# Optimization experiments

Measured on AMD Instinct MI355X. Metric: run time of the kernel, lower is better.

## Reference

```python
import jax, jax.numpy as jnp
import numpy as np

TOPK = 6
E = 512
IN = 384
M = 8192
LN_EPS = 1e-5


def _lin(x, w, b):
    # torch nn.Linear: y = x @ W^T + b, W is [out, in]
    return x @ w.T + b


def setup_inputs() -> dict:
    key = jax.random.key(0)
    ks = jax.random.split(key, 16)
    s = lambda k, sh: (jax.random.normal(k, sh, dtype=jnp.float32) * 0.02)
    return {
        "x": jax.random.normal(ks[0], (1, M, IN), dtype=jnp.float32),
        "fc1_w": s(ks[1], (E, IN)), "fc1_b": jnp.zeros((E,), jnp.float32),
        "wh_w": s(ks[2], (E, E)),   "wh_b": jnp.zeros((E,), jnp.float32),
        "wt_w": s(ks[3], (E, E)),   "wt_b": jnp.zeros((E,), jnp.float32),
        "l1_w": s(ks[4], (E, E)),   "l1_b": jnp.zeros((E,), jnp.float32),
        "l2_w": s(ks[5], (E, E)),   "l2_b": jnp.zeros((E,), jnp.float32),
        "a1_w": s(ks[6], (E // 2, E)), "a1_b": jnp.zeros((E // 2,), jnp.float32),
        "a2_w": s(ks[7], (1, E // 2)), "a2_b": jnp.zeros((1,), jnp.float32),
        "ln_g": jnp.ones((E,), jnp.float32), "ln_b": jnp.zeros((E,), jnp.float32),
    }


def reference(x, fc1_w, fc1_b, wh_w, wh_b, wt_w, wt_b,
              l1_w, l1_b, l2_w, l2_b, a1_w, a1_b, a2_w, a2_b, ln_g, ln_b):
    lrelu = jax.nn.leaky_relu  # slope 0.01 == torch default
    h = lrelu(_lin(x, fc1_w, fc1_b))                      # [B,M,E]
    h = (h + h.mean(axis=1, keepdims=True)) * 0.5
    e_h = _lin(h, wh_w, wh_b)                             # [B,M,E]
    e_t = _lin(h, wt_w, wt_b)                             # [B,M,E]
    scale = E ** (-0.5)
    attn_logit = (e_h * scale) @ jnp.swapaxes(e_t, -2, -1)  # [B,M,M]
    topk_weight, topk_index = jax.lax.top_k(attn_logit, TOPK)  # [B,M,K]
    # gather top-k neighbor tail embeddings: [B,M,K,E]
    Nb_h = jax.vmap(lambda et, idx: et[idx])(e_t, topk_index)
    topk_prob = jax.nn.softmax(topk_weight, axis=2)       # [B,M,K]
    eh_r = topk_prob[..., None] * Nb_h + (1.0 - topk_prob)[..., None] * e_h[:, :, None, :]
    gate = jnp.tanh(e_h[:, :, None, :] + eh_r)            # [B,M,K,E]
    # faithful to torch einsum('ijkl,ijkm->ijk'): sums l and m independently
    ka_weight = Nb_h.sum(axis=-1) * gate.sum(axis=-1)     # [B,M,K]
    ka_prob = jax.nn.softmax(ka_weight, axis=2)           # [B,M,K]
    e_Nh = jnp.einsum('bmk,bmke->bme', ka_prob, Nb_h)     # [B,M,E]
    sum_emb = lrelu(_lin(e_h + e_Nh, l1_w, l1_b))
    bi_emb = lrelu(_lin(e_h * e_Nh, l2_w, l2_b))
    emb = sum_emb + bi_emb                                # [B,M,E] (dropout = eval identity)
    hn = emb[0]                                           # squeeze(0) -> [M,E]
    # GeoGlobalAttention readout: gate_nn = Linear->LeakyReLU->Linear, softmax over nodes
    g = _lin(lrelu(_lin(hn, a1_w, a1_b)), a2_w, a2_b)     # [M,1]
    att = jax.nn.softmax(g, axis=0)
    pooled = (att * hn).sum(axis=0, keepdims=True)        # [1,E]
    mu = pooled.mean(axis=-1, keepdims=True)
    var = jnp.mean((pooled - mu) ** 2, axis=-1, keepdims=True)
    out = (pooled - mu) / jnp.sqrt(var + LN_EPS) * ln_g + ln_b
    return out
```

## Files before the change

kernel.cpp:

```cpp
#include <hip/hip_runtime.h>
#include <math.h>
#include <stdint.h>

#define M_NODES 8192
#define E_DIM   512
#define NTOPK   6
#define ATTN_SCALE 0.04419417382415922f
#define NEG_BIG (-1e38f)
#define CAND_CAP 192

typedef __attribute__((ext_vector_type(8))) short short8;
typedef __attribute__((ext_vector_type(4))) float f32x4;

__device__ __forceinline__ float lrelu(float v) { return v > 0.f ? v : 0.01f * v; }

__device__ __forceinline__ unsigned short f2bf(float f) {
  uint32_t u = __float_as_uint(f);
  uint32_t r = (u + 0x7FFFu + ((u >> 16) & 1u)) >> 16;
  return (unsigned short)r;
}
__device__ __forceinline__ float bf2f(unsigned short s) {
  return __uint_as_float(((uint32_t)s) << 16);
}

__device__ __forceinline__ void async_cp16(const void* gptr, void* lds) {
  auto g1 = reinterpret_cast<const __attribute__((address_space(1))) unsigned int*>(
      reinterpret_cast<uintptr_t>(gptr));
  auto l3 = reinterpret_cast<__attribute__((address_space(3))) unsigned int*>(
      reinterpret_cast<uintptr_t>(lds));
  __builtin_amdgcn_global_load_lds(g1, l3, 16, 0, 0);
}


__global__ __launch_bounds__(256) void wcast_kernel(
    const float* __restrict__ x, const float* __restrict__ fc1w,
    const float* __restrict__ whw, const float* __restrict__ wtw,
    const float* __restrict__ l1w, const float* __restrict__ l2w,
    const float* __restrict__ a1w,
    unsigned short* __restrict__ xT, unsigned short* __restrict__ fc1T,
    unsigned short* __restrict__ whT, unsigned short* __restrict__ wtT,
    unsigned short* __restrict__ l1T, unsigned short* __restrict__ l2T,
    unsigned short* __restrict__ a1T)
{
  const int gid = blockIdx.x * 256 + threadIdx.x;
  const float* src; unsigned short* dst; int K8, local;
  if (gid < 417792) {
    K8 = 48;
    if (gid < 393216) { src = x; dst = xT; local = gid; }
    else { src = fc1w; dst = fc1T; local = gid - 393216; }
  } else {
    K8 = 64;
    if (gid < 450560)      { src = whw; dst = whT; local = gid - 417792; }
    else if (gid < 483328) { src = wtw; dst = wtT; local = gid - 450560; }
    else if (gid < 516096) { src = l1w; dst = l1T; local = gid - 483328; }
    else if (gid < 548864) { src = l2w; dst = l2T; local = gid - 516096; }
    else                   { src = a1w; dst = a1T; local = gid - 548864; }
  }
  const int m = local / K8;
  const int k8 = local - m * K8;
  const float* p = src + (size_t)m * (K8 * 8) + k8 * 8;
  float4 v0 = ((const float4*)p)[0];
  float4 v1 = ((const float4*)p)[1];
  const int Kt = K8 >> 2;
  const size_t ti = ((size_t)(m >> 4) * Kt + (k8 >> 2)) * 512 + ((m & 15) + 16 * (k8 & 3)) * 8;
  uint4 pk;
  pk.x = (uint32_t)f2bf(v0.x) | ((uint32_t)f2bf(v0.y) << 16);
  pk.y = (uint32_t)f2bf(v0.z) | ((uint32_t)f2bf(v0.w) << 16);
  pk.z = (uint32_t)f2bf(v1.x) | ((uint32_t)f2bf(v1.y) << 16);
  pk.w = (uint32_t)f2bf(v1.z) | ((uint32_t)f2bf(v1.w) << 16);
  *(uint4*)(dst + ti) = pk;
}

template <int MODE>
__global__ __launch_bounds__(256) void mfma_gemm(
    const unsigned short* __restrict__ At1, const unsigned short* __restrict__ At2,
    const unsigned short* __restrict__ Wt1, const unsigned short* __restrict__ Wt2,
    const float* __restrict__ b1, const float* __restrict__ b2,
    float* __restrict__ Cf, unsigned short* __restrict__ T1,
    unsigned short* __restrict__ T2, unsigned short* __restrict__ Cbf,
    unsigned short* __restrict__ Cbf2, int N, int K)
{
  __shared__ unsigned short As[2][8 * 512];
  __shared__ unsigned short Bs[2][4 * 512];
  const int Kt = K >> 5;
  const int tid = threadIdx.x, lane = tid & 63, w = tid >> 6;
  const int m0 = blockIdx.y * 128, n0 = blockIdx.x * 64;

  f32x4 acc0[2][4], acc1[2][4];
#pragma unroll
  for (int p = 0; p < 2; p++)
#pragma unroll
    for (int j = 0; j < 4; j++) {
      acc0[p][j] = (f32x4){0.f, 0.f, 0.f, 0.f};
      acc1[p][j] = (f32x4){0.f, 0.f, 0.f, 0.f};
    }

  for (int kt = 0; kt < Kt; kt++) {
    const unsigned short* a1p = At1 + ((size_t)((m0 >> 4) + 2 * w) * Kt + kt) * 512 + lane * 8;
    async_cp16(a1p, &As[0][(2 * w) * 512]);
    async_cp16(a1p + (size_t)Kt * 512, &As[0][(2 * w + 1) * 512]);
    if (MODE == 2) {
      const unsigned short* a2p = At2 + ((size_t)((m0 >> 4) + 2 * w) * Kt + kt) * 512 + lane * 8;
      async_cp16(a2p, &As[1][(2 * w) * 512]);
      async_cp16(a2p + (size_t)Kt * 512, &As[1][(2 * w + 1) * 512]);
    }
    const unsigned short* bp1 = Wt1 + ((size_t)((n0 >> 4) + w) * Kt + kt) * 512 + lane * 8;
    async_cp16(bp1, &Bs[0][w * 512]);
    if (MODE >= 1) {
      const unsigned short* bp2 = Wt2 + ((size_t)((n0 >> 4) + w) * Kt + kt) * 512 + lane * 8;
      async_cp16(bp2, &Bs[1][w * 512]);
    }
    __syncthreads();
    short8 a[2], a2[2], bb[4], bb2[4];
#pragma unroll
    for (int p = 0; p < 2; p++) a[p] = *(const short8*)&As[0][(2 * w + p) * 512 + lane * 8];
    if (MODE == 2) {
#pragma unroll
      for (int p = 0; p < 2; p++) a2[p] = *(const short8*)&As[1][(2 * w + p) * 512 + lane * 8];
    }
#pragma unroll
    for (int j = 0; j < 4; j++) bb[j] = *(const short8*)&Bs[0][j * 512 + lane * 8];
    if (MODE >= 1) {
#pragma unroll
      for (int j = 0; j < 4; j++) bb2[j] = *(const short8*)&Bs[1][j * 512 + lane * 8];
    }
#pragma unroll
    for (int p = 0; p < 2; p++)
#pragma unroll
      for (int j = 0; j < 4; j++) {
        acc0[p][j] = __builtin_amdgcn_mfma_f32_16x16x32_bf16(a[p], bb[j], acc0[p][j], 0, 0, 0);
        if (MODE == 1)
          acc1[p][j] = __builtin_amdgcn_mfma_f32_16x16x32_bf16(a[p], bb2[j], acc1[p][j], 0, 0, 0);
        if (MODE == 2)
          acc1[p][j] = __builtin_amdgcn_mfma_f32_16x16x32_bf16(a2[p], bb2[j], acc1[p][j], 0, 0, 0);
      }
    __syncthreads();
  }

  const int lrow = (lane >> 4) * 4, lcol = lane & 15;
  const int NT = N >> 5;
#pragma unroll
  for (int p = 0; p < 2; p++)
#pragma unroll
    for (int j = 0; j < 4; j++) {
      const int c = n0 + j * 16 + lcol;
      const float bias1 = b1[c];
      const float bias2 = (MODE >= 1) ? b2[c] : 0.f;
#pragma unroll
      for (int d = 0; d < 4; d++) {
        const int r = m0 + w * 32 + p * 16 + lrow + d;
        const float v0 = acc0[p][j][d] + bias1;
        if (MODE == 0) {
          Cf[(size_t)r * N + c] = lrelu(v0);
        } else {
          const size_t ti = ((size_t)(r >> 4) * NT + (c >> 5)) * 512 +
                            ((r & 15) + 16 * ((c >> 3) & 3)) * 8 + (c & 7);
          if (MODE == 1) {
            const float v1 = acc1[p][j][d] + bias2;
            T1[ti] = f2bf(v0);
            T2[ti] = f2bf(v1);
            Cbf[(size_t)r * N + c] = f2bf(v0);
            Cbf2[(size_t)r * N + c] = f2bf(v1);
          } else {
            const float e = lrelu(v0) + lrelu(acc1[p][j][d] + bias2);
            T1[ti] = f2bf(e);
            Cbf[(size_t)r * N + c] = f2bf(e);
          }
        }
      }
    }
}

__global__ __launch_bounds__(256) void colsum_kernel(const float* __restrict__ h,
                                                     float* __restrict__ colsum)
{
  const int t = threadIdx.x;
  const int r0 = blockIdx.x * 128;
  float s0 = 0.f, s1 = 0.f;
  for (int r = 0; r < 128; r++) {
    s0 += h[(size_t)(r0 + r) * E_DIM + t];
    s1 += h[(size_t)(r0 + r) * E_DIM + 256 + t];
  }
  atomicAdd(&colsum[t], s0);
  atomicAdd(&colsum[t + 256], s1);
}

__global__ __launch_bounds__(256) void hupd_cast_kernel(
    const float* __restrict__ h, const float* __restrict__ colsum,
    unsigned short* __restrict__ hT)
{
  const int gid = blockIdx.x * 256 + threadIdx.x;
  const int m = gid >> 6, k8 = gid & 63;
  const float* p = h + (size_t)m * E_DIM + k8 * 8;
  float4 v0 = ((const float4*)p)[0];
  float4 v1 = ((const float4*)p)[1];
  float4 c0 = *(const float4*)(colsum + k8 * 8);
  float4 c1 = *(const float4*)(colsum + k8 * 8 + 4);
  const float im = 1.f / (float)M_NODES;
  v0.x = (v0.x + c0.x * im) * 0.5f; v0.y = (v0.y + c0.y * im) * 0.5f;
  v0.z = (v0.z + c0.z * im) * 0.5f; v0.w = (v0.w + c0.w * im) * 0.5f;
  v1.x = (v1.x + c1.x * im) * 0.5f; v1.y = (v1.y + c1.y * im) * 0.5f;
  v1.z = (v1.z + c1.z * im) * 0.5f; v1.w = (v1.w + c1.w * im) * 0.5f;
  const size_t ti = ((size_t)(m >> 4) * 16 + (k8 >> 2)) * 512 + ((m & 15) + 16 * (k8 & 3)) * 8;
  uint4 pk;
  pk.x = (uint32_t)f2bf(v0.x) | ((uint32_t)f2bf(v0.y) << 16);
  pk.y = (uint32_t)f2bf(v0.z) | ((uint32_t)f2bf(v0.w) << 16);
  pk.z = (uint32_t)f2bf(v1.x) | ((uint32_t)f2bf(v1.y) << 16);
  pk.w = (uint32_t)f2bf(v1.z) | ((uint32_t)f2bf(v1.w) << 16);
  *(uint4*)(hT + ti) = pk;
}

__global__ __launch_bounds__(256) void sgemm_kernel(
    const unsigned short* __restrict__ ehT, const unsigned short* __restrict__ etT,
    unsigned short* __restrict__ sc, float* __restrict__ tmax)
{
  __shared__ unsigned short As[8 * 512];
  __shared__ unsigned short Bs[8 * 512];
  __shared__ unsigned short Sc[128 * 136];
  const int tid = threadIdx.x, lane = tid & 63, w = tid >> 6;
  const int wr = w >> 1, wc = w & 1;
  const int m0 = blockIdx.y * 128;
  const int n0 = blockIdx.x * 128;

  f32x4 acc[4][4];
#pragma unroll
  for (int i = 0; i < 4; i++)
#pragma unroll
    for (int j = 0; j < 4; j++) acc[i][j] = (f32x4){0.f, 0.f, 0.f, 0.f};

  for (int kt = 0; kt < 16; kt++) {
    const int s0 = w, s1 = w + 4;
    async_cp16(ehT + ((size_t)((m0 >> 4) + s0) * 16 + kt) * 512 + lane * 8, &As[s0 * 512]);
    async_cp16(ehT + ((size_t)((m0 >> 4) + s1) * 16 + kt) * 512 + lane * 8, &As[s1 * 512]);
    async_cp16(etT + ((size_t)((n0 >> 4) + s0) * 16 + kt) * 512 + lane * 8, &Bs[s0 * 512]);
    async_cp16(etT + ((size_t)((n0 >> 4) + s1) * 16 + kt) * 512 + lane * 8, &Bs[s1 * 512]);
    __syncthreads();
    short8 a[4], b[4];
#pragma unroll
    for (int i = 0; i < 4; i++) a[i] = *(const short8*)&As[(wr * 4 + i) * 512 + lane * 8];
#pragma unroll
    for (int j = 0; j < 4; j++) b[j] = *(const short8*)&Bs[(wc * 4 + j) * 512 + lane * 8];
#pragma unroll
    for (int i = 0; i < 4; i++)
#pragma unroll
      for (int j = 0; j < 4; j++)
        acc[i][j] = __builtin_amdgcn_mfma_f32_16x16x32_bf16(a[i], b[j], acc[i][j], 0, 0, 0);
    __syncthreads();
  }

  const int lrow = (lane >> 4) * 4, lcol = lane & 15;
#pragma unroll
  for (int i = 0; i < 4; i++) {
    const int row = wr * 64 + i * 16 + lrow;
#pragma unroll
    for (int j = 0; j < 4; j++) {
      const int col = wc * 64 + j * 16 + lcol;
      Sc[(row + 0) * 136 + col] = f2bf(acc[i][j][0]);
      Sc[(row + 1) * 136 + col] = f2bf(acc[i][j][1]);
      Sc[(row + 2) * 136 + col] = f2bf(acc[i][j][2]);
      Sc[(row + 3) * 136 + col] = f2bf(acc[i][j][3]);
    }
  }
  __syncthreads();

  const int row = tid >> 1, half = tid & 1;
  const unsigned short* src = &Sc[row * 136 + half * 64];
  unsigned short* dst = sc + (size_t)(m0 + row) * M_NODES + n0 + half * 64;
  float mx = NEG_BIG;
#pragma unroll
  for (int q = 0; q < 8; q++) {
    short8 s8 = *(const short8*)(src + q * 8);
    *(short8*)(dst + q * 8) = s8;
#pragma unroll
    for (int e = 0; e < 8; e++) mx = fmaxf(mx, bf2f((unsigned short)s8[e]));
  }
  tmax[(size_t)(m0 + row) * 128 + blockIdx.x * 2 + half] = mx;
}

__global__ __launch_bounds__(256) void scan_topk_kernel(
    const unsigned short* __restrict__ sc, const float* __restrict__ tmax,
    float* __restrict__ tkv, int* __restrict__ tki)
{
  __shared__ float cv[4][CAND_CAP];
  __shared__ int   ci[4][CAND_CAP];
  __shared__ int   cnt[4];
  const int lane = threadIdx.x & 63;
  const int w = threadIdx.x >> 6;
  const int row = blockIdx.x * 4 + w;
  if (lane == 0) cnt[w] = 0;
  __syncthreads();

  const float* tm = tmax + (size_t)row * 128;
  const float v2 = fmaxf(tm[lane], tm[lane + 64]);
  uint32_t u = __float_as_uint(v2);
  u = ((int)u >= 0) ? (u | 0x80000000u) : ~u;
  uint32_t key = (u & ~63u) | (uint32_t)lane;
  float tau = 0.f;
#pragma unroll
  for (int it = 0; it < 6; it++) {
    uint32_t k = key;
#pragma unroll
    for (int off = 32; off; off >>= 1) {
      const uint32_t o = (uint32_t)__shfl_xor((int)k, off);
      k = k > o ? k : o;
    }
    const int wl = (int)(k & 63u);
    if (it == 5) tau = __shfl(v2, wl);
    if (lane == wl) key = 0u;
  }

  const unsigned short* rp = sc + (size_t)row * M_NODES;
  for (int g = 0; g < 16; g++) {
    const int base = (g * 64 + lane) * 8;
    short8 s8 = *(const short8*)(rp + base);
#pragma unroll
    for (int e = 0; e < 8; e++) {
      const float f = bf2f((unsigned short)s8[e]);
      if (f >= tau) {
        const int slot = atomicAdd(&cnt[w], 1);
        if (slot < CAND_CAP) { cv[w][slot] = f; ci[w][slot] = base + e; }
      }
    }
  }

  int n = cnt[w];
  n = n < CAND_CAP ? n : CAND_CAP;
  for (int c = lane; c < n; c += 64) {
    const float v = cv[w][c];
    const int idx = ci[w][c];
    int rank = 0;
    for (int j = 0; j < n; j++) {
      const float vj = cv[w][j];
      rank += (vj > v) || (vj == v && ci[w][j] < idx);
    }
    if (rank < NTOPK) {
      const size_t base = (size_t)row * NTOPK + rank;
      tkv[base] = v * ATTN_SCALE;
      tki[base] = idx;
    }
  }
}

__global__ __launch_bounds__(256) void combine_kernel(
    const unsigned short* __restrict__ ehRow, const unsigned short* __restrict__ etRow,
    const float* __restrict__ tkv, const int* __restrict__ tki,
    unsigned short* __restrict__ s1T, unsigned short* __restrict__ s2T)
{
  const int lane = threadIdx.x & 63;
  const int m = blockIdx.x * 4 + (threadIdx.x >> 6);

  float wv[NTOPK]; int id[NTOPK];
#pragma unroll
  for (int k = 0; k < NTOPK; k++) {
    wv[k] = tkv[(size_t)m * NTOPK + k];
    id[k] = tki[(size_t)m * NTOPK + k];
  }

  float mx = wv[0];
#pragma unroll
  for (int k = 1; k < NTOPK; k++) mx = fmaxf(mx, wv[k]);
  float p[NTOPK]; float s = 0.f;
#pragma unroll
  for (int k = 0; k < NTOPK; k++) { p[k] = expf(wv[k] - mx); s += p[k]; }
  const float inv = 1.f / s;
#pragma unroll
  for (int k = 0; k < NTOPK; k++) p[k] *= inv;

  short8 eh8 = *(const short8*)(ehRow + (size_t)m * E_DIM + lane * 8);
  float ehv[8];
#pragma unroll
  for (int e = 0; e < 8; e++) ehv[e] = bf2f((unsigned short)eh8[e]);

  float nv[NTOPK][8];
#pragma unroll
  for (int k = 0; k < NTOPK; k++) {
    short8 nb = *(const short8*)(etRow + (size_t)id[k] * E_DIM + lane * 8);
#pragma unroll
    for (int e = 0; e < 8; e++) nv[k][e] = bf2f((unsigned short)nb[e]);
  }

  float ka[NTOPK];
#pragma unroll
  for (int k = 0; k < NTOPK; k++) {
    float snb = 0.f, sg = 0.f;
    const float aa = 2.f - p[k], bb = p[k];
#pragma unroll
    for (int e = 0; e < 8; e++) {
      snb += nv[k][e];
      sg += tanhf(fmaf(aa, ehv[e], bb * nv[k][e]));
    }
#pragma unroll
    for (int off = 32; off; off >>= 1) {
      snb += __shfl_xor(snb, off);
      sg += __shfl_xor(sg, off);
    }
    ka[k] = snb * sg;
  }
  float km = ka[0];
#pragma unroll
  for (int k = 1; k < NTOPK; k++) km = fmaxf(km, ka[k]);
  float kp[NTOPK]; float ks = 0.f;
#pragma unroll
  for (int k = 0; k < NTOPK; k++) { kp[k] = expf(ka[k] - km); ks += kp[k]; }
  const float kinv = 1.f / ks;

  const size_t tbase = ((size_t)(m >> 4) * 16 + (lane >> 2)) * 512 +
                       ((m & 15) + 16 * (lane & 3)) * 8;
  unsigned short o1[8], o2[8];
#pragma unroll
  for (int e = 0; e < 8; e++) {
    float o = 0.f;
#pragma unroll
    for (int k = 0; k < NTOPK; k++) o = fmaf(kp[k], nv[k][e], o);
    o *= kinv;
    o1[e] = f2bf(ehv[e] + o);
    o2[e] = f2bf(ehv[e] * o);
  }
  *(short8*)(s1T + tbase) = *(short8*)o1;
  *(short8*)(s2T + tbase) = *(short8*)o2;
}

__global__ __launch_bounds__(256) void gate_g_kernel(
    const float* __restrict__ ahid, const float* __restrict__ a2w,
    const float* __restrict__ a2b, float* __restrict__ g)
{
  const int lane = threadIdx.x & 63;
  const int m = blockIdx.x * 4 + (threadIdx.x >> 6);
  float s = 0.f;
  for (int j = lane; j < 256; j += 64)
    s = fmaf(a2w[j], ahid[(size_t)m * 256 + j], s);
#pragma unroll
  for (int off = 32; off; off >>= 1) s += __shfl_xor(s, off);
  if (lane == 0) g[m] = s + a2b[0];
}

__global__ __launch_bounds__(1024) void softmax_stats_kernel(
    const float* __restrict__ g, float* __restrict__ stats)
{
  __shared__ float red[16];
  __shared__ float red2[16];
  const int t = threadIdx.x;
  float mx = NEG_BIG;
  for (int i = t; i < M_NODES; i += 1024) mx = fmaxf(mx, g[i]);
#pragma unroll
  for (int off = 32; off; off >>= 1) mx = fmaxf(mx, __shfl_xor(mx, off));
  if ((t & 63) == 0) red[t >> 6] = mx;
  __syncthreads();
  float gmx = red[0];
  for (int i = 1; i < 16; i++) gmx = fmaxf(gmx, red[i]);
  float s = 0.f;
  for (int i = t; i < M_NODES; i += 1024) s += expf(g[i] - gmx);
#pragma unroll
  for (int off = 32; off; off >>= 1) s += __shfl_xor(s, off);
  if ((t & 63) == 0) red2[t >> 6] = s;
  __syncthreads();
  if (t == 0) {
    float tot = 0.f;
    for (int i = 0; i < 16; i++) tot += red2[i];
    stats[0] = gmx; stats[1] = tot;
  }
}

__global__ __launch_bounds__(256) void pooled_kernel(
    const unsigned short* __restrict__ emb, const float* __restrict__ g,
    const float* __restrict__ stats, float* __restrict__ pooled)
{
  const int t = threadIdx.x;
  const int r0 = blockIdx.x * 128;
  const float mx = stats[0];
  const float inv = 1.f / stats[1];
  float a0 = 0.f, a1 = 0.f;
  for (int r = 0; r < 128; r++) {
    const int m = r0 + r;
    const float wv = expf(g[m] - mx) * inv;
    a0 = fmaf(wv, bf2f(emb[(size_t)m * E_DIM + t]), a0);
    a1 = fmaf(wv, bf2f(emb[(size_t)m * E_DIM + 256 + t]), a1);
  }
  atomicAdd(&pooled[t], a0);
  atomicAdd(&pooled[t + 256], a1);
}

__global__ __launch_bounds__(512) void ln_kernel(
    const float* __restrict__ pooled, const float* __restrict__ lng,
    const float* __restrict__ lnb, float* __restrict__ out)
{
  __shared__ float red[8];
  __shared__ float red2[8];
  const int t = threadIdx.x;
  const float v = pooled[t];
  float s = v;
#pragma unroll
  for (int off = 32; off; off >>= 1) s += __shfl_xor(s, off);
  if ((t & 63) == 0) red[t >> 6] = s;
  __syncthreads();
  float tot = 0.f;
  for (int i = 0; i < 8; i++) tot += red[i];
  const float mu = tot / (float)E_DIM;
  const float d = v - mu;
  float q = d * d;
#pragma unroll
  for (int off = 32; off; off >>= 1) q += __shfl_xor(q, off);
  if ((t & 63) == 0) red2[t >> 6] = q;
  __syncthreads();
  float vt = 0.f;
  for (int i = 0; i < 8; i++) vt += red2[i];
  const float var = vt / (float)E_DIM;
  out[t] = d * rsqrtf(var + 1e-5f) * lng[t] + lnb[t];
}

extern "C" void kernel_launch(void* const* d_in, const int* in_sizes, int n_in,
                              void* d_out, int out_size, void* d_ws, size_t ws_size,
                              hipStream_t stream)
{
  const float* x     = (const float*)d_in[0];
  const float* fc1_w = (const float*)d_in[1];
  const float* fc1_b = (const float*)d_in[2];
  const float* wh_w  = (const float*)d_in[3];
  const float* wh_b  = (const float*)d_in[4];
  const float* wt_w  = (const float*)d_in[5];
  const float* wt_b  = (const float*)d_in[6];
  const float* l1_w  = (const float*)d_in[7];
  const float* l1_b  = (const float*)d_in[8];
  const float* l2_w  = (const float*)d_in[9];
  const float* l2_b  = (const float*)d_in[10];
  const float* a1_w  = (const float*)d_in[11];
  const float* a1_b  = (const float*)d_in[12];
  const float* a2_w  = (const float*)d_in[13];
  const float* a2_b  = (const float*)d_in[14];
  const float* ln_g  = (const float*)d_in[15];
  const float* ln_b  = (const float*)d_in[16];

  char* ws = (char*)d_ws;
  const size_t MiB = 1 << 20;
  unsigned short* fc1T = (unsigned short*)(ws + 0);
  unsigned short* whT  = (unsigned short*)(ws + 393216);
  unsigned short* wtT  = (unsigned short*)(ws + 917504);
  unsigned short* l1T  = (unsigned short*)(ws + 1441792);
  unsigned short* l2T  = (unsigned short*)(ws + 1966080);
  unsigned short* a1T  = (unsigned short*)(ws + 2490368);
  unsigned short* xT     = (unsigned short*)(ws + 3 * MiB);
  float*          h      = (float*)(ws + 9 * MiB);
  unsigned short* hT     = (unsigned short*)(ws + 25 * MiB);
  unsigned short* ehT    = (unsigned short*)(ws + 33 * MiB);
  unsigned short* etT    = (unsigned short*)(ws + 41 * MiB);
  unsigned short* ehRow  = (unsigned short*)(ws + 49 * MiB);
  unsigned short* etRow  = (unsigned short*)(ws + 57 * MiB);
  float*          tmaxb  = (float*)(ws + 65 * MiB);
  unsigned short* s1T    = (unsigned short*)(ws + 3 * MiB);
  unsigned short* s2T    = (unsigned short*)(ws + 11 * MiB);
  unsigned short* embT   = (unsigned short*)(ws + 19 * MiB);
  unsigned short* embRow = (unsigned short*)(ws + 27 * MiB);
  float*          ahid   = (float*)(ws + 41 * MiB);
  unsigned short* scores = (unsigned short*)(ws + 96 * MiB);
  char*           smal   = ws + 69 * MiB;
  float* tkv    = (float*)(smal);
  int*   tki    = (int*)(smal + 196608);
  float* colsum = (float*)(smal + 393216);
  float* g      = (float*)(smal + 395264);
  float* stats  = (float*)(smal + 428032);
  float* pooled = (float*)(smal + 432128);

  hipMemsetAsync(smal + 393216, 0, 43008, stream);

  wcast_kernel<<<2208, 256, 0, stream>>>(x, fc1_w, wh_w, wt_w, l1_w, l2_w, a1_w,
                                         xT, fc1T, whT, wtT, l1T, l2T, a1T);
  mfma_gemm<0><<<dim3(8, 64), 256, 0, stream>>>(
      xT, nullptr, fc1T, nullptr, fc1_b, nullptr, h, nullptr, nullptr, nullptr, nullptr,
      512, 384);
  colsum_kernel<<<64, 256, 0, stream>>>(h, colsum);
  hupd_cast_kernel<<<2048, 256, 0, stream>>>(h, colsum, hT);
  mfma_gemm<1><<<dim3(8, 64), 256, 0, stream>>>(
      hT, nullptr, whT, wtT, wh_b, wt_b, nullptr, ehT, etT, ehRow, etRow, 512, 512);
  sgemm_kernel<<<dim3(64, 64), 256, 0, stream>>>(ehT, etT, scores, tmaxb);
  scan_topk_kernel<<<M_NODES / 4, 256, 0, stream>>>(scores, tmaxb, tkv, tki);
  combine_kernel<<<M_NODES / 4, 256, 0, stream>>>(ehRow, etRow, tkv, tki, s1T, s2T);
  mfma_gemm<2><<<dim3(8, 64), 256, 0, stream>>>(
      s1T, s2T, l1T, l2T, l1_b, l2_b, nullptr, embT, nullptr, embRow, nullptr, 512, 512);
  mfma_gemm<0><<<dim3(4, 64), 256, 0, stream>>>(
      embT, nullptr, a1T, nullptr, a1_b, nullptr, ahid, nullptr, nullptr, nullptr, nullptr,
      256, 512);
  gate_g_kernel<<<M_NODES / 4, 256, 0, stream>>>(ahid, a2_w, a2_b, g);
  softmax_stats_kernel<<<1, 1024, 0, stream>>>(g, stats);
  pooled_kernel<<<64, 256, 0, stream>>>(embRow, g, stats, pooled);
  ln_kernel<<<1, 512, 0, stream>>>(pooled, ln_g, ln_b, (float*)d_out);
}
```

Baseline: 357.7 us.

## Store score tiles in MFMA fragment layout and scan them block-wise for top-k

The score GEMM now writes each bf16 output fragment straight from registers into a tiled, fragment-ordered layout, dropping the LDS staging buffer and its extra barrier. Row maxima are computed with lane shuffles. The top-k scan kernel is restructured so each block handles four rows that share fragment storage, and it decodes column indices from the tiled layout. The memset now also zeroes the top-k buffers. This aims to cut LDS traffic and raise occupancy in the score GEMM, at the cost of a more complex index mapping and candidate-slot atomics shared across the four waves.

Measured after the change: 338.0 us. 5.5% less time.

```diff
diff --git a/kernel.cpp b/kernel.cpp
--- a/kernel.cpp
+++ b/kernel.cpp
@@ -30,6 +30,7 @@
       reinterpret_cast<uintptr_t>(lds));
   __builtin_amdgcn_global_load_lds(g1, l3, 16, 0, 0);
 }
+
 
 
 __global__ __launch_bounds__(256) void wcast_kernel(
@@ -216,7 +217,6 @@
 {
   __shared__ unsigned short As[8 * 512];
   __shared__ unsigned short Bs[8 * 512];
-  __shared__ unsigned short Sc[128 * 136];
   const int tid = threadIdx.x, lane = tid & 63, w = tid >> 6;
   const int wr = w >> 1, wc = w & 1;
   const int m0 = blockIdx.y * 128;
@@ -248,33 +248,48 @@
     __syncthreads();
   }
 
-  const int lrow = (lane >> 4) * 4, lcol = lane & 15;
-#pragma unroll
-  for (int i = 0; i < 4; i++) {
-    const int row = wr * 64 + i * 16 + lrow;
-#pragma unroll
-    for (int j = 0; j < 4; j++) {
-      const int col = wc * 64 + j * 16 + lcol;
-      Sc[(row + 0) * 136 + col] = f2bf(acc[i][j][0]);
-      Sc[(row + 1) * 136 + col] = f2bf(acc[i][j][1]);
-      Sc[(row + 2) * 136 + col] = f2bf(acc[i][j][2]);
-      Sc[(row + 3) * 136 + col] = f2bf(acc[i][j][3]);
-    }
-  }
-  __syncthreads();
-
-  const int row = tid >> 1, half = tid & 1;
-  const unsigned short* src = &Sc[row * 136 + half * 64];
-  unsigned short* dst = sc + (size_t)(m0 + row) * M_NODES + n0 + half * 64;
-  float mx = NEG_BIG;
-#pragma unroll
-  for (int q = 0; q < 8; q++) {
-    short8 s8 = *(const short8*)(src + q * 8);
-    *(short8*)(dst + q * 8) = s8;
-#pragma unroll
-    for (int e = 0; e < 8; e++) mx = fmaxf(mx, bf2f((unsigned short)s8[e]));
-  }
-  tmax[(size_t)(m0 + row) * 128 + blockIdx.x * 2 + half] = mx;
+  const int q = lane >> 4, lcol = lane & 15;
+  const size_t blkbase = ((size_t)blockIdx.y * 64 + blockIdx.x) * 16384;
+
+  float rm[4][4];
+#pragma unroll
+  for (int i = 0; i < 4; i++)
+#pragma unroll
+    for (int d = 0; d < 4; d++) rm[i][d] = NEG_BIG;
+
+#pragma unroll
+  for (int i = 0; i < 4; i++)
+#pragma unroll
+    for (int jj = 0; jj < 2; jj++) {
+      unsigned short o[8];
+#pragma unroll
+      for (int d = 0; d < 4; d++) {
+        o[d] = f2bf(acc[i][2 * jj][d]);
+        o[4 + d] = f2bf(acc[i][2 * jj + 1][d]);
+        rm[i][d] = fmaxf(rm[i][d], fmaxf(bf2f(o[d]), bf2f(o[4 + d])));
+      }
+      const size_t off = blkbase + (size_t)(wr * 4 + i) * 2048 + q * 512 +
+                         (wc * 32 + jj * 16 + lcol) * 8;
+      *(short8*)(sc + off) = *(short8*)o;
+    }
+
+#pragma unroll
+  for (int i = 0; i < 4; i++)
+#pragma unroll
+    for (int d = 0; d < 4; d++) {
+#pragma unroll
+      for (int off = 1; off < 16; off <<= 1)
+        rm[i][d] = fmaxf(rm[i][d], __shfl_xor(rm[i][d], off));
+    }
+
+  if (lcol == 0) {
+#pragma unroll
+    for (int i = 0; i < 4; i++)
+#pragma unroll
+      for (int d = 0; d < 4; d++)
+        tmax[(size_t)(m0 + wr * 64 + i * 16 + q * 4 + d) * 128 +
+             blockIdx.x * 2 + wc] = rm[i][d];
+  }
 }
 
 __global__ __launch_bounds__(256) void scan_topk_kernel(
@@ -284,44 +299,63 @@
   __shared__ float cv[4][CAND_CAP];
   __shared__ int   ci[4][CAND_CAP];
   __shared__ int   cnt[4];
-  const int lane = threadIdx.x & 63;
-  const int w = threadIdx.x >> 6;
-  const int row = blockIdx.x * 4 + w;
-  if (lane == 0) cnt[w] = 0;
+  __shared__ float taus[4];
+  const int tid = threadIdx.x;
+  const int lane = tid & 63;
+  const int w = tid >> 6;
+  const int rg = blockIdx.x;
+  const int bm = rg >> 5;
+  const int g = rg & 31;
+  const int wr = g >> 4, gi = (g >> 2) & 3, gq = g & 3;
+  const int r0 = bm * 128 + wr * 64 + gi * 16 + gq * 4;
+
+  if (tid < 4) cnt[tid] = 0;
+
+  {
+    const float* tm = tmax + (size_t)(r0 + w) * 128;
+    const float v2 = fmaxf(tm[lane], tm[lane + 64]);
+    uint32_t u = __float_as_uint(v2);
+    u = ((int)u >= 0) ? (u | 0x80000000u) : ~u;
+    uint32_t key = (u & ~63u) | (uint32_t)lane;
+    float tau = 0.f;
+#pragma unroll
+    for (int it = 0; it < 6; it++) {
+      uint32_t k = key;
+#pragma unroll
+      for (int off = 32; off; off >>= 1) {
+        const uint32_t o = (uint32_t)__shfl_xor((int)k, off);
+        k = k > o ? k : o;
+      }
+      const int wl = (int)(k & 63u);
+      if (it == 5) tau = __shfl(v2, wl);
+      if (lane == wl) key = 0u;
+    }
+    if (lane == 0) taus[w] = tau;
+  }
   __syncthreads();
-
-  const float* tm = tmax + (size_t)row * 128;
-  const float v2 = fmaxf(tm[lane], tm[lane + 64]);
-  uint32_t u = __float_as_uint(v2);
-  u = ((int)u >= 0) ? (u | 0x80000000u) : ~u;
-  uint32_t key = (u & ~63u) | (uint32_t)lane;
-  float tau = 0.f;
-#pragma unroll
-  for (int it = 0; it < 6; it++) {
-    uint32_t k = key;
-#pragma unroll
-    for (int off = 32; off; off >>= 1) {
-      const uint32_t o = (uint32_t)__shfl_xor((int)k, off);
-      k = k > o ? k : o;
-    }
-    const int wl = (int)(k & 63u);
-    if (it == 5) tau = __shfl(v2, wl);
-    if (lane == wl) key = 0u;
-  }
-
-  const unsigned short* rp = sc + (size_t)row * M_NODES;
-  for (int g = 0; g < 16; g++) {
-    const int base = (g * 64 + lane) * 8;
-    short8 s8 = *(const short8*)(rp + base);
+  const float t0 = taus[0], t1 = taus[1], t2 = taus[2], t3 = taus[3];
+
+  const size_t rowoff = (size_t)(wr * 4 + gi) * 2048 + gq * 512 + lane * 8;
+  const int colbase = (lane >> 5) * 64 + 2 * ((lane >> 4) & 1) * 16 + (lane & 15);
+  for (int t = 0; t < 16; t++) {
+    const int bn = w * 16 + t;
+    short8 u = *(const short8*)(sc + ((size_t)(bm * 64 + bn)) * 16384 + rowoff);
+    const int cb = bn * 128 + colbase;
 #pragma unroll
     for (int e = 0; e < 8; e++) {
-      const float f = bf2f((unsigned short)s8[e]);
+      const float f = bf2f((unsigned short)u[e]);
+      const int d = e & 3;
+      const float tau = (d == 0) ? t0 : (d == 1) ? t1 : (d == 2) ? t2 : t3;
       if (f >= tau) {
-        const int slot = atomicAdd(&cnt[w], 1);
-        if (slot < CAND_CAP) { cv[w][slot] = f; ci[w][slot] = base + e; }
+        const int slot = atomicAdd(&cnt[d], 1);
+        if (slot < CAND_CAP) {
+          cv[d][slot] = f;
+          ci[d][slot] = cb + (e >> 2) * 16;
+        }
       }
     }
   }
+  __syncthreads();
 
   int n = cnt[w];
   n = n < CAND_CAP ? n : CAND_CAP;
@@ -334,7 +368,7 @@
       rank += (vj > v) || (vj == v && ci[w][j] < idx);
     }
     if (rank < NTOPK) {
-      const size_t base = (size_t)row * NTOPK + rank;
+      const size_t base = (size_t)(r0 + w) * NTOPK + rank;
       tkv[base] = v * ATTN_SCALE;
       tki[base] = idx;
     }
@@ -560,7 +594,7 @@
   float* stats  = (float*)(smal + 428032);
   float* pooled = (float*)(smal + 432128);
 
-  hipMemsetAsync(smal + 393216, 0, 43008, stream);
+  hipMemsetAsync(smal, 0, 436224, stream);
 
   wcast_kernel<<<2208, 256, 0, stream>>>(x, fc1_w, wh_w, wt_w, l1_w, l2_w, a1_w,
                                          xT, fc1T, whT, wtT, l1T, l2T, a1T);
```
